# Optimization experiments

Hardware: AMD Instinct MI355X
Metric: run time of the kernel (lower is better)

## Reference

```python
import jax, jax.numpy as jnp
import numpy as np
from jax import lax

B, T = 2, 2048
D = 512        # d_model
K = 64         # k_lookback (causal window)


def setup_inputs() -> dict:
    key = jax.random.key(0)
    k1, k2, k3 = jax.random.split(key, 3)
    x = jax.random.normal(k1, (B, 1, T), jnp.float32)
    conv_w = jax.random.normal(k2, (D, 1, 3), jnp.float32) * 0.2
    conv_b = jax.random.normal(k3, (D,), jnp.float32) * 0.05
    gate = jnp.array(0.5, jnp.float32)  # nn.Parameter scalar
    return {"x": x, "conv_w": conv_w, "conv_b": conv_b, "gate": gate}


def reference(x, conv_w, conv_b, gate):
    # feature_proj: Conv1d(1, D, k=3, pad=1) + exact GELU (dropout inactive at eval)
    q = lax.conv_general_dilated(
        x, conv_w, window_strides=(1,), padding=[(1, 1)],
        dimension_numbers=("NCH", "OIH", "NCH"))
    q = jax.nn.gelu(q + conv_b[None, :, None], approximate=False)  # [B, D, T]

    # causal sliding windows: keys_windows[b,c,t,j] = q[b,c, t-(K-1)+j] (0 outside)
    padded = jnp.pad(q, ((0, 0), (0, 0), (K - 1, 0)))
    idx = jnp.arange(T)[:, None] + jnp.arange(K)[None, :]  # [T, K]
    kw = padded[:, :, idx]                                  # [B, D, T, K]

    energy = jnp.einsum("bct,bctk->btk", q, kw)             # [B, T, K]
    attn = jax.nn.softmax(energy / np.float32(np.sqrt(D)), axis=-1)
    context = jnp.einsum("btk,bctk->bct", attn, kw)         # [B, D, T]
    return context * jnp.tanh(gate)
```

## Files before the change

### kernel.cpp

```cpp
#include <hip/hip_runtime.h>
#include <math.h>

#define B 2
#define T 2048
#define D 512
#define KW 64
#define SCALE 0.044194173824159216f

typedef __attribute__((ext_vector_type(8))) short short8;
typedef __attribute__((ext_vector_type(4))) float f32x4;

__device__ __forceinline__ ushort f2bf(float f) {
  union { float f; unsigned u; } v; v.f = f;
  unsigned r = v.u + 0x7fffu + ((v.u >> 16) & 1u);
  return (ushort)(r >> 16);
}

__global__ __launch_bounds__(256) void k_conv(
    const float* __restrict__ x, const float* __restrict__ w,
    const float* __restrict__ bias, ushort* __restrict__ q,
    ushort* __restrict__ qT) {
  __shared__ float s_tile[64 * 65];

  int blk = blockIdx.x;
  int b   = blk >> 8;
  int rem = blk & 255;
  int t0  = (rem >> 3) << 6;
  int c0  = (rem & 7) << 6;
  int tid = threadIdx.x;

  int lt = tid >> 2;
  int cb = (tid & 3) << 4;
  int t = t0 + lt;
  float xm1 = (t > 0)     ? x[b * T + t - 1] : 0.f;
  float x0  =               x[b * T + t];
  float xp1 = (t < T - 1) ? x[b * T + t + 1] : 0.f;
#pragma unroll
  for (int e = 0; e < 16; ++e) {
    int c = c0 + cb + e;
    float v = xm1 * w[c * 3] + x0 * w[c * 3 + 1] + xp1 * w[c * 3 + 2] + bias[c];
    float g = 0.5f * v * (1.f + erff(v * 0.70710678118654752f));
    q[((size_t)b * T + t) * D + c] = f2bf(g);
    s_tile[lt * 65 + cb + e] = g;
  }
  __syncthreads();

  int lc = tid >> 2;
  int tb = (tid & 3) << 4;
#pragma unroll
  for (int e = 0; e < 16; ++e) {
    int ltt = tb + e;
    qT[((size_t)b * D + c0 + lc) * T + t0 + ltt] = f2bf(s_tile[ltt * 65 + lc]);
  }
}

__global__ __launch_bounds__(256) void k_attn(
    const ushort* __restrict__ q, const ushort* __restrict__ qT,
    const float* __restrict__ gate, float* __restrict__ out) {
  __shared__ float s_E[3 * 5 * 4 * 64];
  __shared__ alignas(16) ushort s_attn[16 * 96];

  int blk  = blockIdx.x;
  int tile = (blk & 7) * 32 + (blk >> 3);
  int b  = tile >> 7;
  int t0 = (tile & 127) << 4;
  int tid  = threadIdx.x;
  int wv   = tid >> 6;
  int lane = tid & 63;
  int n    = lane & 15;
  int quad = lane >> 4;

  const ushort* qb = q + (size_t)b * T * D;
  const short8 zero8 = {0, 0, 0, 0, 0, 0, 0, 0};

  f32x4 acc[5];
#pragma unroll
  for (int jc = 0; jc < 5; ++jc) acc[jc] = (f32x4){0.f, 0.f, 0.f, 0.f};

#pragma unroll
  for (int i = 0; i < 4; ++i) {
    int cofs = (wv * 4 + i) * 32 + quad * 8;
    short8 afr = *(const short8*)(qb + (size_t)(t0 + n) * D + cofs);
#pragma unroll
    for (int jc = 0; jc < 5; ++jc) {
      int tp = t0 - (KW - 1) + jc * 16 + n;
      short8 bfr = (tp >= 0 && tp < T)
                       ? *(const short8*)(qb + (size_t)tp * D + cofs)
                       : zero8;
      acc[jc] = __builtin_amdgcn_mfma_f32_16x16x32_bf16(afr, bfr, acc[jc], 0, 0, 0);
    }
  }

  if (wv) {
#pragma unroll
    for (int jc = 0; jc < 5; ++jc)
#pragma unroll
      for (int r = 0; r < 4; ++r)
        s_E[(((wv - 1) * 5 + jc) * 4 + r) * 64 + lane] = acc[jc][r];
  }
  __syncthreads();

  if (wv == 0) {
#pragma unroll
    for (int ww = 0; ww < 3; ++ww)
#pragma unroll
      for (int jc = 0; jc < 5; ++jc)
#pragma unroll
        for (int r = 0; r < 4; ++r)
          acc[jc][r] += s_E[((ww * 5 + jc) * 4 + r) * 64 + lane];

#pragma unroll
    for (int r = 0; r < 4; ++r) {
      int m = quad * 4 + r;
      float e[5];
      float mx = -1e30f;
#pragma unroll
      for (int jc = 0; jc < 5; ++jc) {
        int j = jc * 16 + n;
        bool valid = (j >= m) && (j <= m + (KW - 1));
        e[jc] = valid ? acc[jc][r] * SCALE : -1e30f;
        mx = fmaxf(mx, e[jc]);
      }
#pragma unroll
      for (int off = 1; off <= 8; off <<= 1) mx = fmaxf(mx, __shfl_xor(mx, off, 64));
      float p[5];
      float s = 0.f;
#pragma unroll
      for (int jc = 0; jc < 5; ++jc) {
        p[jc] = (e[jc] > -1e29f) ? __expf(e[jc] - mx) : 0.f;
        s += p[jc];
      }
#pragma unroll
      for (int off = 1; off <= 8; off <<= 1) s += __shfl_xor(s, off, 64);
      float inv = 1.f / s;
#pragma unroll
      for (int jc = 0; jc < 5; ++jc) {
        int j = jc * 16 + n;
        s_attn[m * 96 + j + 1] = f2bf(p[jc] * inv);
      }
      int jp = (n == 0) ? 0 : (80 + n);
      s_attn[m * 96 + jp] = 0;
    }
  }
  __syncthreads();

  short8 afr2[3];
#pragma unroll
  for (int ks = 0; ks < 3; ++ks)
    afr2[ks] = *(const short8*)(s_attn + n * 96 + ks * 32 + quad * 8);

  const ushort* qTb = qT + (size_t)b * D * T;
  const float tg = tanhf(gate[0]);

#pragma unroll
  for (int ncl = 0; ncl < 8; ++ncl) {
    int c = (wv * 8 + ncl) * 16 + n;
    f32x4 co = (f32x4){0.f, 0.f, 0.f, 0.f};
#pragma unroll
    for (int ks = 0; ks < 3; ++ks) {
      int tbase = t0 - KW + ks * 32 + quad * 8;
      short8 bfr = (tbase >= 0 && tbase < T)
                       ? *(const short8*)(qTb + (size_t)c * T + tbase)
                       : zero8;
      co = __builtin_amdgcn_mfma_f32_16x16x32_bf16(afr2[ks], bfr, co, 0, 0, 0);
    }
    f32x4 o;
    o[0] = co[0] * tg; o[1] = co[1] * tg; o[2] = co[2] * tg; o[3] = co[3] * tg;
    *(f32x4*)(out + ((size_t)b * D + c) * T + t0 + quad * 4) = o;
  }
}

extern "C" void kernel_launch(void* const* d_in, const int* in_sizes, int n_in,
                              void* d_out, int out_size, void* d_ws, size_t ws_size,
                              hipStream_t stream) {
  const float* x      = (const float*)d_in[0];
  const float* conv_w = (const float*)d_in[1];
  const float* conv_b = (const float*)d_in[2];
  const float* gate   = (const float*)d_in[3];
  float* out = (float*)d_out;

  ushort* q_ws  = (ushort*)d_ws;
  ushort* qT_ws = q_ws + (size_t)B * T * D;

  k_conv<<<B * 256, 256, 0, stream>>>(x, conv_w, conv_b, q_ws, qT_ws);
  k_attn<<<B * T / 16, 256, 0, stream>>>(q_ws, qT_ws, gate, out);
}
```

Baseline: 83.98 us.

## Zero-pad q/qT workspaces, batch loads before MFMA, replicate softmax per wave

Adds zero-padded halos to the q and qT workspaces, written by 8 extra blocks in the conv kernel, so the attention kernel can drop its boundary checks. All operand fragments for both MFMA stages are now loaded up front to raise memory-level parallelism. Every wave now reduces the partial energies and computes the softmax redundantly into its own LDS buffer, which removes the second block barrier and the single-wave serial section. The cost is higher register pressure from the batched fragments and duplicated softmax work across waves.

```diff
diff --git a/kernel.cpp b/kernel.cpp
--- a/kernel.cpp
+++ b/kernel.cpp
@@ -7,6 +7,9 @@
 #define KW 64
 #define SCALE 0.044194173824159216f
 
+#define RQ (64 + T + 16)
+#define TTP (64 + T + 16)
+
 typedef __attribute__((ext_vector_type(8))) short short8;
 typedef __attribute__((ext_vector_type(4))) float f32x4;
 
@@ -20,14 +23,44 @@
     const float* __restrict__ x, const float* __restrict__ w,
     const float* __restrict__ bias, ushort* __restrict__ q,
     ushort* __restrict__ qT) {
+  int blk = blockIdx.x;
+  int tid = threadIdx.x;
+
+  if (blk >= 512) {
+    int ztid = (blk - 512) * 256 + tid;
+    const uint4 z = {0u, 0u, 0u, 0u};
+    for (int task = ztid; task < 20480; task += 2048) {
+      size_t e;
+      if (task < 8192) {
+        int b = task >> 12, i = task & 4095;
+        e = (size_t)b * RQ * D + (size_t)i * 8;
+      } else if (task < 10240) {
+        int idx = task - 8192;
+        int b = idx >> 10, i = idx & 1023;
+        e = (size_t)b * RQ * D + (size_t)(64 + T) * D + (size_t)i * 8;
+      } else if (task < 18432) {
+        int idx = task - 10240;
+        int r = idx >> 3, i = idx & 7;
+        e = (size_t)r * TTP + (size_t)i * 8;
+        *(uint4*)(qT + e) = z;
+        continue;
+      } else {
+        int idx = task - 18432;
+        int r = idx >> 1, i = idx & 1;
+        e = (size_t)r * TTP + 64 + T + (size_t)i * 8;
+        *(uint4*)(qT + e) = z;
+        continue;
+      }
+      *(uint4*)(q + e) = z;
+    }
+    return;
+  }
+
   __shared__ float s_tile[64 * 65];
-
-  int blk = blockIdx.x;
   int b   = blk >> 8;
   int rem = blk & 255;
   int t0  = (rem >> 3) << 6;
   int c0  = (rem & 7) << 6;
-  int tid = threadIdx.x;
 
   int lt = tid >> 2;
   int cb = (tid & 3) << 4;
@@ -40,7 +73,7 @@
     int c = c0 + cb + e;
     float v = xm1 * w[c * 3] + x0 * w[c * 3 + 1] + xp1 * w[c * 3 + 2] + bias[c];
     float g = 0.5f * v * (1.f + erff(v * 0.70710678118654752f));
-    q[((size_t)b * T + t) * D + c] = f2bf(g);
+    q[((size_t)b * RQ + 64 + t) * D + c] = f2bf(g);
     s_tile[lt * 65 + cb + e] = g;
   }
   __syncthreads();
@@ -50,15 +83,16 @@
 #pragma unroll
   for (int e = 0; e < 16; ++e) {
     int ltt = tb + e;
-    qT[((size_t)b * D + c0 + lc) * T + t0 + ltt] = f2bf(s_tile[ltt * 65 + lc]);
+    qT[((size_t)b * D + c0 + lc) * TTP + 64 + t0 + ltt] =
+        f2bf(s_tile[ltt * 65 + lc]);
   }
 }
 
 __global__ __launch_bounds__(256) void k_attn(
     const ushort* __restrict__ q, const ushort* __restrict__ qT,
     const float* __restrict__ gate, float* __restrict__ out) {
-  __shared__ float s_E[3 * 5 * 4 * 64];
-  __shared__ alignas(16) ushort s_attn[16 * 96];
+  __shared__ float s_E[4 * 5 * 4 * 64];
+  __shared__ alignas(16) ushort s_attn[4][16 * 96];
 
   int blk  = blockIdx.x;
   int tile = (blk & 7) * 32 + (blk >> 3);
@@ -70,100 +104,106 @@
   int n    = lane & 15;
   int quad = lane >> 4;
 
-  const ushort* qb = q + (size_t)b * T * D;
-  const short8 zero8 = {0, 0, 0, 0, 0, 0, 0, 0};
-
-  f32x4 acc[5];
-#pragma unroll
-  for (int jc = 0; jc < 5; ++jc) acc[jc] = (f32x4){0.f, 0.f, 0.f, 0.f};
-
+  const ushort* qb = q + (size_t)b * RQ * D + (size_t)64 * D;
+  const ushort* qTb = qT + (size_t)b * D * TTP;
+
+  short8 afr[4], bfr[4][5];
 #pragma unroll
   for (int i = 0; i < 4; ++i) {
     int cofs = (wv * 4 + i) * 32 + quad * 8;
-    short8 afr = *(const short8*)(qb + (size_t)(t0 + n) * D + cofs);
+    afr[i] = *(const short8*)(qb + (size_t)(t0 + n) * D + cofs);
 #pragma unroll
     for (int jc = 0; jc < 5; ++jc) {
       int tp = t0 - (KW - 1) + jc * 16 + n;
-      short8 bfr = (tp >= 0 && tp < T)
-                       ? *(const short8*)(qb + (size_t)tp * D + cofs)
-                       : zero8;
-      acc[jc] = __builtin_amdgcn_mfma_f32_16x16x32_bf16(afr, bfr, acc[jc], 0, 0, 0);
-    }
-  }
-
-  if (wv) {
+      bfr[i][jc] = *(const short8*)(qb + (ptrdiff_t)tp * D + cofs);
+    }
+  }
+
+  f32x4 acc[5];
+#pragma unroll
+  for (int jc = 0; jc < 5; ++jc) acc[jc] = (f32x4){0.f, 0.f, 0.f, 0.f};
+#pragma unroll
+  for (int i = 0; i < 4; ++i)
 #pragma unroll
     for (int jc = 0; jc < 5; ++jc)
+      acc[jc] = __builtin_amdgcn_mfma_f32_16x16x32_bf16(afr[i], bfr[i][jc],
+                                                        acc[jc], 0, 0, 0);
+
+#pragma unroll
+  for (int jc = 0; jc < 5; ++jc)
+#pragma unroll
+    for (int r = 0; r < 4; ++r)
+      s_E[((wv * 5 + jc) * 4 + r) * 64 + lane] = acc[jc][r];
+  __syncthreads();
+
+#pragma unroll
+  for (int ww = 0; ww < 4; ++ww) {
+    if (ww == wv) continue;
+#pragma unroll
+    for (int jc = 0; jc < 5; ++jc)
 #pragma unroll
       for (int r = 0; r < 4; ++r)
-        s_E[(((wv - 1) * 5 + jc) * 4 + r) * 64 + lane] = acc[jc][r];
-  }
-  __syncthreads();
-
-  if (wv == 0) {
-#pragma unroll
-    for (int ww = 0; ww < 3; ++ww)
-#pragma unroll
-      for (int jc = 0; jc < 5; ++jc)
-#pragma unroll
-        for (int r = 0; r < 4; ++r)
-          acc[jc][r] += s_E[((ww * 5 + jc) * 4 + r) * 64 + lane];
-
-#pragma unroll
-    for (int r = 0; r < 4; ++r) {
-      int m = quad * 4 + r;
-      float e[5];
-      float mx = -1e30f;
-#pragma unroll
-      for (int jc = 0; jc < 5; ++jc) {
-        int j = jc * 16 + n;
-        bool valid = (j >= m) && (j <= m + (KW - 1));
-        e[jc] = valid ? acc[jc][r] * SCALE : -1e30f;
-        mx = fmaxf(mx, e[jc]);
-      }
-#pragma unroll
-      for (int off = 1; off <= 8; off <<= 1) mx = fmaxf(mx, __shfl_xor(mx, off, 64));
-      float p[5];
-      float s = 0.f;
-#pragma unroll
-      for (int jc = 0; jc < 5; ++jc) {
-        p[jc] = (e[jc] > -1e29f) ? __expf(e[jc] - mx) : 0.f;
-        s += p[jc];
-      }
-#pragma unroll
-      for (int off = 1; off <= 8; off <<= 1) s += __shfl_xor(s, off, 64);
-      float inv = 1.f / s;
-#pragma unroll
-      for (int jc = 0; jc < 5; ++jc) {
-        int j = jc * 16 + n;
-        s_attn[m * 96 + j + 1] = f2bf(p[jc] * inv);
-      }
-      int jp = (n == 0) ? 0 : (80 + n);
-      s_attn[m * 96 + jp] = 0;
-    }
-  }
-  __syncthreads();
+        acc[jc][r] += s_E[((ww * 5 + jc) * 4 + r) * 64 + lane];
+  }
+
+  ushort* sa = s_attn[wv];
+#pragma unroll
+  for (int r = 0; r < 4; ++r) {
+    int m = quad * 4 + r;
+    float e[5];
+    float mx = -1e30f;
+#pragma unroll
+    for (int jc = 0; jc < 5; ++jc) {
+      int j = jc * 16 + n;
+      bool valid = (j >= m) && (j <= m + (KW - 1));
+      e[jc] = valid ? acc[jc][r] * SCALE : -1e30f;
+      mx = fmaxf(mx, e[jc]);
+    }
+#pragma unroll
+    for (int off = 1; off <= 8; off <<= 1) mx = fmaxf(mx, __shfl_xor(mx, off, 64));
+    float p[5];
+    float s = 0.f;
+#pragma unroll
+    for (int jc = 0; jc < 5; ++jc) {
+      p[jc] = (e[jc] > -1e29f) ? __expf(e[jc] - mx) : 0.f;
+      s += p[jc];
+    }
+#pragma unroll
+    for (int off = 1; off <= 8; off <<= 1) s += __shfl_xor(s, off, 64);
+    float inv = 1.f / s;
+#pragma unroll
+    for (int jc = 0; jc < 5; ++jc) {
+      int j = jc * 16 + n;
+      sa[m * 96 + j + 1] = f2bf(p[jc] * inv);
+    }
+    int jp = (n == 0) ? 0 : (80 + n);
+    sa[m * 96 + jp] = 0;
+  }
 
   short8 afr2[3];
 #pragma unroll
   for (int ks = 0; ks < 3; ++ks)
-    afr2[ks] = *(const short8*)(s_attn + n * 96 + ks * 32 + quad * 8);
-
-  const ushort* qTb = qT + (size_t)b * D * T;
+    afr2[ks] = *(const short8*)(sa + n * 96 + ks * 32 + quad * 8);
+
+  short8 bfr2[8][3];
+#pragma unroll
+  for (int ncl = 0; ncl < 8; ++ncl) {
+    int c = (wv * 8 + ncl) * 16 + n;
+#pragma unroll
+    for (int ks = 0; ks < 3; ++ks) {
+      bfr2[ncl][ks] = *(const short8*)(qTb + (size_t)c * TTP + t0 + ks * 32 + quad * 8);
+    }
+  }
+
   const float tg = tanhf(gate[0]);
-
 #pragma unroll
   for (int ncl = 0; ncl < 8; ++ncl) {
     int c = (wv * 8 + ncl) * 16 + n;
     f32x4 co = (f32x4){0.f, 0.f, 0.f, 0.f};
 #pragma unroll
-    for (int ks = 0; ks < 3; ++ks) {
-      int tbase = t0 - KW + ks * 32 + quad * 8;
-      short8 bfr = (tbase >= 0 && tbase < T)
-                       ? *(const short8*)(qTb + (size_t)c * T + tbase)
-                       : zero8;
-      co = __builtin_amdgcn_mfma_f32_16x16x32_bf16(afr2[ks], bfr, co, 0, 0, 0);
-    }
+    for (int ks = 0; ks < 3; ++ks)
+      co = __builtin_amdgcn_mfma_f32_16x16x32_bf16(afr2[ks], bfr2[ncl][ks],
+                                                   co, 0, 0, 0);
     f32x4 o;
     o[0] = co[0] * tg; o[1] = co[1] * tg; o[2] = co[2] * tg; o[3] = co[3] * tg;
     *(f32x4*)(out + ((size_t)b * D + c) * T + t0 + quad * 4) = o;
@@ -180,8 +220,8 @@
   float* out = (float*)d_out;
 
   ushort* q_ws  = (ushort*)d_ws;
-  ushort* qT_ws = q_ws + (size_t)B * T * D;
-
-  k_conv<<<B * 256, 256, 0, stream>>>(x, conv_w, conv_b, q_ws, qT_ws);
+  ushort* qT_ws = q_ws + (size_t)B * RQ * D;
+
+  k_conv<<<520, 256, 0, stream>>>(x, conv_w, conv_b, q_ws, qT_ws);
   k_attn<<<B * T / 16, 256, 0, stream>>>(q_ws, qT_ws, gate, out);
 }
```

New measurement: 79.67 us. 5.1% less time.

## Fuse conv+GELU into attention kernel, recomputing q in registers per tile

Applied to the files above, without the earlier changes.

Drops the separate conv/GELU kernel and its bf16 q/qT workspace. Each attention block now recomputes the 80-row window of conv+GELU outputs in registers. The A-operand for the energy MFMA comes from lane shuffles, and the context B-operand is transposed through a per-wave LDS band staged in three steps. GELU switches from erf to a tanh-form approximation using exp2/rcp intrinsics. This removes the global round-trip and one launch, at the cost of roughly 5x redundant GELU compute, a slightly different GELU approximation, and one-block-per-CU launch bounds.

```diff
diff --git a/kernel.cpp b/kernel.cpp
--- a/kernel.cpp
+++ b/kernel.cpp
@@ -9,6 +9,7 @@
 
 typedef __attribute__((ext_vector_type(8))) short short8;
 typedef __attribute__((ext_vector_type(4))) float f32x4;
+typedef __attribute__((ext_vector_type(4))) int   i32x4;
 
 __device__ __forceinline__ ushort f2bf(float f) {
   union { float f; unsigned u; } v; v.f = f;
@@ -16,48 +17,21 @@
   return (ushort)(r >> 16);
 }
 
-__global__ __launch_bounds__(256) void k_conv(
+__device__ __forceinline__ float gelu_fast(float v) {
+  float v2 = v * v;
+  float u  = fmaf(v2 * v, 0.03567740814f, 0.7978845608f * v);
+  float e  = __builtin_amdgcn_exp2f(2.885390082f * u);
+  float r  = __builtin_amdgcn_rcpf(1.f + e);
+  return fmaf(-v, r, v);
+}
+
+__global__ __launch_bounds__(256, 1) void k_fused(
     const float* __restrict__ x, const float* __restrict__ w,
-    const float* __restrict__ bias, ushort* __restrict__ q,
-    ushort* __restrict__ qT) {
-  __shared__ float s_tile[64 * 65];
-
-  int blk = blockIdx.x;
-  int b   = blk >> 8;
-  int rem = blk & 255;
-  int t0  = (rem >> 3) << 6;
-  int c0  = (rem & 7) << 6;
-  int tid = threadIdx.x;
-
-  int lt = tid >> 2;
-  int cb = (tid & 3) << 4;
-  int t = t0 + lt;
-  float xm1 = (t > 0)     ? x[b * T + t - 1] : 0.f;
-  float x0  =               x[b * T + t];
-  float xp1 = (t < T - 1) ? x[b * T + t + 1] : 0.f;
-#pragma unroll
-  for (int e = 0; e < 16; ++e) {
-    int c = c0 + cb + e;
-    float v = xm1 * w[c * 3] + x0 * w[c * 3 + 1] + xp1 * w[c * 3 + 2] + bias[c];
-    float g = 0.5f * v * (1.f + erff(v * 0.70710678118654752f));
-    q[((size_t)b * T + t) * D + c] = f2bf(g);
-    s_tile[lt * 65 + cb + e] = g;
-  }
-  __syncthreads();
-
-  int lc = tid >> 2;
-  int tb = (tid & 3) << 4;
-#pragma unroll
-  for (int e = 0; e < 16; ++e) {
-    int ltt = tb + e;
-    qT[((size_t)b * D + c0 + lc) * T + t0 + ltt] = f2bf(s_tile[ltt * 65 + lc]);
-  }
-}
-
-__global__ __launch_bounds__(256) void k_attn(
-    const ushort* __restrict__ q, const ushort* __restrict__ qT,
-    const float* __restrict__ gate, float* __restrict__ out) {
-  __shared__ float s_E[3 * 5 * 4 * 64];
+    const float* __restrict__ bias, const float* __restrict__ gate,
+    float* __restrict__ out) {
+  __shared__ float s_x[84];
+  __shared__ alignas(16) ushort s_band[4][32 * 128];
+  __shared__ alignas(16) f32x4 s_E[3][5][64];
   __shared__ alignas(16) ushort s_attn[16 * 96];
 
   int blk  = blockIdx.x;
@@ -70,33 +44,78 @@
   int n    = lane & 15;
   int quad = lane >> 4;
 
-  const ushort* qb = q + (size_t)b * T * D;
-  const short8 zero8 = {0, 0, 0, 0, 0, 0, 0, 0};
+  if (tid < 82) {
+    int tx = t0 - 64 + tid;
+    s_x[tid] = (tx >= 0 && tx < T) ? x[b * T + tx] : 0.f;
+  }
+  __syncthreads();
+
+  float xv[5][3];
+  bool vrow[5];
+#pragma unroll
+  for (int jc = 0; jc < 5; ++jc) {
+    int idx = 16 * jc + n + 1;
+    xv[jc][0] = s_x[idx - 1];
+    xv[jc][1] = s_x[idx];
+    xv[jc][2] = s_x[idx + 1];
+    int rowt = t0 - 63 + 16 * jc + n;
+    vrow[jc] = (rowt >= 0) && (rowt < T);
+  }
+
+  short8 bfr[4][5];
+#pragma unroll
+  for (int i = 0; i < 4; ++i) {
+    int c0g = wv * 128 + i * 32 + quad * 8;
+    float wreg[24], breg[8];
+#pragma unroll
+    for (int v4 = 0; v4 < 6; ++v4)
+      *(float4*)&wreg[v4 * 4] = *(const float4*)(w + (size_t)c0g * 3 + v4 * 4);
+    *(float4*)&breg[0] = *(const float4*)(bias + c0g);
+    *(float4*)&breg[4] = *(const float4*)(bias + c0g + 4);
+#pragma unroll
+    for (int jc = 0; jc < 5; ++jc) {
+      short8 h;
+#pragma unroll
+      for (int e = 0; e < 8; ++e) {
+        float val = fmaf(xv[jc][0], wreg[e * 3],
+                    fmaf(xv[jc][1], wreg[e * 3 + 1],
+                    fmaf(xv[jc][2], wreg[e * 3 + 2], breg[e])));
+        float g = vrow[jc] ? gelu_fast(val) : 0.f;
+        h[e] = (short)f2bf(g);
+      }
+      bfr[i][jc] = h;
+    }
+  }
+
+  int src = (lane & 48) | ((n + 15) & 15);
+  short8 afr[4];
+#pragma unroll
+  for (int i = 0; i < 4; ++i) {
+    i32x4 v4 = *(i32x4*)&bfr[i][4];
+    i32x4 v3 = *(i32x4*)&bfr[i][3];
+    i32x4 p;
+#pragma unroll
+    for (int k = 0; k < 4; ++k) {
+      int a4 = __shfl(v4[k], src, 64);
+      int a3 = __shfl(v3[k], src, 64);
+      p[k] = (n == 0) ? a3 : a4;
+    }
+    afr[i] = *(short8*)&p;
+  }
 
   f32x4 acc[5];
 #pragma unroll
   for (int jc = 0; jc < 5; ++jc) acc[jc] = (f32x4){0.f, 0.f, 0.f, 0.f};
-
-#pragma unroll
-  for (int i = 0; i < 4; ++i) {
-    int cofs = (wv * 4 + i) * 32 + quad * 8;
-    short8 afr = *(const short8*)(qb + (size_t)(t0 + n) * D + cofs);
-#pragma unroll
-    for (int jc = 0; jc < 5; ++jc) {
-      int tp = t0 - (KW - 1) + jc * 16 + n;
-      short8 bfr = (tp >= 0 && tp < T)
-                       ? *(const short8*)(qb + (size_t)tp * D + cofs)
-                       : zero8;
-      acc[jc] = __builtin_amdgcn_mfma_f32_16x16x32_bf16(afr, bfr, acc[jc], 0, 0, 0);
-    }
-  }
+#pragma unroll
+  for (int i = 0; i < 4; ++i)
+#pragma unroll
+    for (int jc = 0; jc < 5; ++jc)
+      acc[jc] = __builtin_amdgcn_mfma_f32_16x16x32_bf16(afr[i], bfr[i][jc],
+                                                        acc[jc], 0, 0, 0);
 
   if (wv) {
 #pragma unroll
-    for (int jc = 0; jc < 5; ++jc)
-#pragma unroll
-      for (int r = 0; r < 4; ++r)
-        s_E[(((wv - 1) * 5 + jc) * 4 + r) * 64 + lane] = acc[jc][r];
+    for (int jc = 0; jc < 5; ++jc) s_E[wv - 1][jc][lane] = acc[jc];
   }
   __syncthreads();
 
@@ -104,11 +123,11 @@
 #pragma unroll
     for (int ww = 0; ww < 3; ++ww)
 #pragma unroll
-      for (int jc = 0; jc < 5; ++jc)
-#pragma unroll
-        for (int r = 0; r < 4; ++r)
-          acc[jc][r] += s_E[((ww * 5 + jc) * 4 + r) * 64 + lane];
-
+      for (int jc = 0; jc < 5; ++jc) {
+        f32x4 v = s_E[ww][jc][lane];
+        acc[jc][0] += v[0]; acc[jc][1] += v[1];
+        acc[jc][2] += v[2]; acc[jc][3] += v[3];
+      }
 #pragma unroll
     for (int r = 0; r < 4; ++r) {
       int m = quad * 4 + r;
@@ -142,6 +161,47 @@
       s_attn[m * 96 + jp] = 0;
     }
   }
+
+  ushort* slab = s_band[wv];
+  const short8 zero8 = {0, 0, 0, 0, 0, 0, 0, 0};
+
+#define WRITE_BAND(KS)                                                        \
+  {                                                                           \
+    _Pragma("unroll")                                                         \
+    for (int i = 0; i < 4; ++i) {                \
+      int wp = n + 1;                                                         \
+      int off = wp * 128 + ((i * 32 + quad * 8 + 16 * (wp >> 3)) & 127);      \
+      *(short8*)(slab + off) = bfr[i][2 * (KS)];                              \
+    }                                                                         \
+    if (n == 15) {                                              \
+      _Pragma("unroll")                                                       \
+      for (int i = 0; i < 4; ++i) {                                           \
+        int off = (i * 32 + quad * 8) & 127;                                  \
+        *(short8*)(slab + off) = ((KS) == 0) ? zero8 : bfr[i][2 * (KS) - 1];  \
+      }                                                                       \
+    }                                                                         \
+    if (n <= 14) {                                           \
+      _Pragma("unroll")                                                       \
+      for (int i = 0; i < 4; ++i) {                                           \
+        int wp = 17 + n;                                                      \
+        int off = wp * 128 + ((i * 32 + quad * 8 + 16 * (wp >> 3)) & 127);    \
+        *(short8*)(slab + off) = ((KS) == 2) ? zero8 : bfr[i][2 * (KS) + 1];  \
+      }                                                                       \
+    }                                                                         \
+  }
+
+#define GATHER_B2(dst, NCL)                                                   \
+  {                                                                           \
+    const ushort* gp = slab + quad * 8 * 128 +                                \
+                       (((NCL) * 16 + n + 16 * quad) & 127);                  \
+    _Pragma("unroll")                                                         \
+    for (int jj = 0; jj < 8; ++jj) (dst)[jj] = (short)gp[jj * 128];           \
+  }
+
+  WRITE_BAND(0)
+  short8 b2pre[8];
+#pragma unroll
+  for (int ncl = 0; ncl < 8; ++ncl) GATHER_B2(b2pre[ncl], ncl)
   __syncthreads();
 
   short8 afr2[3];
@@ -149,23 +209,39 @@
   for (int ks = 0; ks < 3; ++ks)
     afr2[ks] = *(const short8*)(s_attn + n * 96 + ks * 32 + quad * 8);
 
-  const ushort* qTb = qT + (size_t)b * D * T;
+  f32x4 co[8];
+#pragma unroll
+  for (int ncl = 0; ncl < 8; ++ncl) {
+    co[ncl] = (f32x4){0.f, 0.f, 0.f, 0.f};
+    co[ncl] = __builtin_amdgcn_mfma_f32_16x16x32_bf16(afr2[0], b2pre[ncl],
+                                                      co[ncl], 0, 0, 0);
+  }
+
+  WRITE_BAND(1)
+#pragma unroll
+  for (int ncl = 0; ncl < 8; ++ncl) {
+    short8 b2;
+    GATHER_B2(b2, ncl)
+    co[ncl] = __builtin_amdgcn_mfma_f32_16x16x32_bf16(afr2[1], b2,
+                                                      co[ncl], 0, 0, 0);
+  }
+
+  WRITE_BAND(2)
+#pragma unroll
+  for (int ncl = 0; ncl < 8; ++ncl) {
+    short8 b2;
+    GATHER_B2(b2, ncl)
+    co[ncl] = __builtin_amdgcn_mfma_f32_16x16x32_bf16(afr2[2], b2,
+                                                      co[ncl], 0, 0, 0);
+  }
+
   const float tg = tanhf(gate[0]);
-
 #pragma unroll
   for (int ncl = 0; ncl < 8; ++ncl) {
     int c = (wv * 8 + ncl) * 16 + n;
-    f32x4 co = (f32x4){0.f, 0.f, 0.f, 0.f};
-#pragma unroll
-    for (int ks = 0; ks < 3; ++ks) {
-      int tbase = t0 - KW + ks * 32 + quad * 8;
-      short8 bfr = (tbase >= 0 && tbase < T)
-                       ? *(const short8*)(qTb + (size_t)c * T + tbase)
-                       : zero8;
-      co = __builtin_amdgcn_mfma_f32_16x16x32_bf16(afr2[ks], bfr, co, 0, 0, 0);
-    }
     f32x4 o;
-    o[0] = co[0] * tg; o[1] = co[1] * tg; o[2] = co[2] * tg; o[3] = co[3] * tg;
+    o[0] = co[ncl][0] * tg; o[1] = co[ncl][1] * tg;
+    o[2] = co[ncl][2] * tg; o[3] = co[ncl][3] * tg;
     *(f32x4*)(out + ((size_t)b * D + c) * T + t0 + quad * 4) = o;
   }
 }
@@ -179,9 +255,5 @@
   const float* gate   = (const float*)d_in[3];
   float* out = (float*)d_out;
 
-  ushort* q_ws  = (ushort*)d_ws;
-  ushort* qT_ws = q_ws + (size_t)B * T * D;
-
-  k_conv<<<B * 256, 256, 0, stream>>>(x, conv_w, conv_b, q_ws, qT_ws);
-  k_attn<<<B * T / 16, 256, 0, stream>>>(q_ws, qT_ws, gate, out);
-}
+  k_fused<<<B * T / 16, 256, 0, stream>>>(x, conv_w, conv_b, gate, out);
+}
```

Measured after the change: 76.38 us. 1.1x faster.
